# Performance work log

Measured on AMD Instinct MI355X. Metric: run time of the kernel, lower is better.

## Reference

```python
import jax, jax.numpy as jnp
import numpy as np


def _gcn_conv(x, W, b, src, dst, n):
    # PyG GCNConv: add self-loops, symmetric normalization deg^{-1/2} A deg^{-1/2},
    # linear transform, scatter-add aggregation, bias.
    h = x @ W  # [N, H]
    # degree including self-loop (count of dst occurrences + 1)
    deg = jnp.zeros((n,), h.dtype).at[dst].add(1.0) + 1.0
    dinv = jax.lax.rsqrt(deg)  # deg^{-1/2}
    edge_norm = (dinv[src] * dinv[dst])[:, None]  # [E, 1]
    agg = jax.ops.segment_sum(h[src] * edge_norm, dst, num_segments=n)  # [N, H]
    # self-loop contribution: norm = dinv[i]*dinv[i]
    return agg + h * (dinv * dinv)[:, None] + b


def setup_inputs() -> dict:
    N, E, F_IN, HID, OUT = 100000, 1600000, 128, 128, 64
    key = jax.random.key(0)
    ks = jax.random.split(key, 8)
    x = jax.random.normal(ks[0], (N, F_IN), dtype=jnp.float32)
    edge_index = jax.random.randint(ks[1], (2, E), 0, N, dtype=jnp.int32)
    s1 = 1.0 / np.sqrt(F_IN)
    s2 = 1.0 / np.sqrt(HID)
    W1 = jax.random.uniform(ks[2], (F_IN, HID), jnp.float32, -s1, s1)
    b1 = jax.random.uniform(ks[3], (HID,), jnp.float32, -s1, s1)
    W2 = jax.random.uniform(ks[4], (HID, HID), jnp.float32, -s2, s2)
    b2 = jax.random.uniform(ks[5], (HID,), jnp.float32, -s2, s2)
    W_out = jax.random.uniform(ks[6], (HID, OUT), jnp.float32, -s2, s2)
    b_out = jax.random.uniform(ks[7], (OUT,), jnp.float32, -s2, s2)
    return {"x": x, "edge_index": edge_index, "W1": W1, "b1": b1,
            "W2": W2, "b2": b2, "W_out": W_out, "b_out": b_out}


def reference(x, edge_index, W1, b1, W2, b2, W_out, b_out):
    n = x.shape[0]
    src, dst = edge_index[0], edge_index[1]
    h = _gcn_conv(x, W1, b1, src, dst, n)
    h = jax.nn.relu(h)
    # F.dropout(training=self.training): identity in eval mode
    h = _gcn_conv(h, W2, b2, src, dst, n)
    h = jax.nn.relu(h)
    logits = h @ W_out + b_out
    return jax.nn.log_softmax(logits, axis=1)
```

## Files before the change

### kernel.cpp

```cpp
#include <hip/hip_runtime.h>
#include <hip/hip_bf16.h>


#define FEAT 128
#define OUTF 64
#define BSH 7
#define BNODES (1 << BSH)
#define SCHUNK_SH 12
#define SCHUNK (1 << SCHUNK_SH)
#define NREP 8
#define GDEPTH 16

typedef __attribute__((ext_vector_type(8))) short short8;
typedef __attribute__((ext_vector_type(4))) float f32x4;

__device__ __forceinline__ unsigned short bf16_rn(float f) {
    unsigned int u = __float_as_uint(f);
    u += 0x7FFFu + ((u >> 16) & 1u);
    return (unsigned short)(u >> 16);
}
__device__ __forceinline__ float bf16_lo(unsigned int u) { return __uint_as_float(u << 16); }
__device__ __forceinline__ float bf16_hi(unsigned int u) { return __uint_as_float(u & 0xFFFF0000u); }

__global__ __launch_bounds__(256) void bincount8_kernel(
        const int* __restrict__ dst, int* __restrict__ bcnt8, int E, int NB) {
    __shared__ int h[8192];
    int t = threadIdx.x;
    int nb8 = NB * NREP;
    for (int i = t; i < nb8; i += 256) h[i] = 0;
    __syncthreads();
    int stride = gridDim.x * 256;
    for (int e = blockIdx.x * 256 + t; e < E; e += stride) {
        int rep = (e >> SCHUNK_SH) & (NREP - 1);
        atomicAdd(&h[((dst[e] >> BSH) << 3) | rep], 1);
    }
    __syncthreads();
    for (int i = t; i < nb8; i += 256)
        if (h[i]) atomicAdd(&bcnt8[i], h[i]);
}

__global__ __launch_bounds__(1024) void bucket_scan8_kernel(
        const int* __restrict__ bcnt8, int* __restrict__ bcur8,
        int* __restrict__ bbase, int NB, int E) {
    int t = threadIdx.x;
    int nb8 = NB * NREP;
    int base = t * 8;
    int v[8];
    #pragma unroll
    for (int i = 0; i < 8; ++i) v[i] = (base + i < nb8) ? bcnt8[base + i] : 0;
    int local = 0;
    #pragma unroll
    for (int i = 0; i < 8; ++i) local += v[i];
    int lane = t & 63, wv = t >> 6;
    int x = local;
    #pragma unroll
    for (int o = 1; o < 64; o <<= 1) {
        int y = __shfl_up(x, o);
        if (lane >= o) x += y;
    }
    __shared__ int wsum[16];
    if (lane == 63) wsum[wv] = x;
    __syncthreads();
    int woff = 0;
    for (int i = 0; i < wv; ++i) woff += wsum[i];
    int run = woff + x - local;
    #pragma unroll
    for (int i = 0; i < 8; ++i) {
        int g = base + i;
        if (g < nb8) {
            bcur8[g] = run;
            if ((g & (NREP - 1)) == 0) bbase[g >> 3] = run;
        }
        run += v[i];
    }
    if (t == 0) bbase[NB] = E;
}

__global__ __launch_bounds__(256) void bin_scatter_kernel(
        const int* __restrict__ src, const int* __restrict__ dst,
        int* __restrict__ bcur8, unsigned int* __restrict__ staged,
        int E, int NB) {
    __shared__ int lcnt[1024];
    __shared__ int lbase[1024];
    int t = threadIdx.x;
    int rep = blockIdx.x & (NREP - 1);
    int e0 = blockIdx.x << SCHUNK_SH;
    int e1 = min(e0 + SCHUNK, E);
    for (int i = t; i < NB; i += 256) lcnt[i] = 0;
    __syncthreads();
    for (int e = e0 + t; e < e1; e += 256)
        atomicAdd(&lcnt[dst[e] >> BSH], 1);
    __syncthreads();
    for (int i = t; i < NB; i += 256) {
        int c = lcnt[i];
        lbase[i] = c ? atomicAdd(&bcur8[(i << 3) | rep], c) : 0;
        lcnt[i] = 0;
    }
    __syncthreads();
    for (int e = e0 + t; e < e1; e += 256) {
        int s = src[e], d = dst[e];
        int b = d >> BSH, dl = d & (BNODES - 1);
        int pos = lbase[b] + atomicAdd(&lcnt[b], 1);
        staged[pos] = (unsigned int)s | ((unsigned int)dl << 25);
    }
}

__global__ __launch_bounds__(256) void bucket_place_kernel(
        const unsigned int* __restrict__ staged, const int* __restrict__ bbase,
        int* __restrict__ row_ptr, float* __restrict__ dinv,
        int* __restrict__ csr_src, int N, int E) {
    int b = blockIdx.x;
    int t = threadIdx.x;
    int base = bbase[b], end = bbase[b + 1];
    __shared__ int cnt[BNODES];
    __shared__ int cur[BNODES];
    __shared__ int wsum2[2];
    if (t < BNODES) cnt[t] = 0;
    __syncthreads();
    for (int i = base + t; i < end; i += 256)
        atomicAdd(&cnt[staged[i] >> 25], 1);
    __syncthreads();

    bool act = t < BNODES;
    int v = act ? cnt[t] : 0;
    int lane = t & 63, wv = t >> 6;
    int x = v;
    #pragma unroll
    for (int o = 1; o < 64; o <<= 1) {
        int y = __shfl_up(x, o);
        if (lane >= o) x += y;
    }
    if (lane == 63 && wv == 0) wsum2[0] = x;
    __syncthreads();
    if (act) {
        int excl = x - v + (wv == 1 ? wsum2[0] : 0);
        int gnode = b * BNODES + t;
        int rp = base + excl;
        cur[t] = rp;
        if (gnode < N) {
            row_ptr[gnode] = rp;
            dinv[gnode] = rsqrtf((float)v + 1.0f);
        }
    }
    __syncthreads();
    for (int i = base + t; i < end; i += 256) {
        unsigned int u = staged[i];
        int dl = u >> 25;
        int p = atomicAdd(&cur[dl], 1);
        csr_src[p] = (int)(u & 0x1FFFFFFu);
    }
    if (b == 0 && t == 0) row_ptr[N] = E;
}

__global__ __launch_bounds__(256) void convw_kernel(
        const float* __restrict__ W1, const float* __restrict__ W2,
        const float* __restrict__ Wout,
        __hip_bfloat16* __restrict__ W1t, __hip_bfloat16* __restrict__ W2t,
        __hip_bfloat16* __restrict__ WoutT) {
    int idx = blockIdx.x * 256 + threadIdx.x;
    if (idx < 2 * FEAT * FEAT) {
        int which = idx >> 14;
        int r = idx & (FEAT * FEAT - 1);
        int n = r >> 7, k = r & 127;
        const float* W = which ? W2 : W1;
        unsigned short* Wt = (unsigned short*)(which ? W2t : W1t);
        Wt[r] = bf16_rn(W[k * FEAT + n]);
    } else if (idx < 2 * FEAT * FEAT + OUTF * FEAT) {
        int r = idx - 2 * FEAT * FEAT;
        int n = r >> 7, k = r & 127;
        ((unsigned short*)WoutT)[r] = bf16_rn(Wout[k * OUTF + n]);
    }
}

template <bool IN_FP32>
__global__ __launch_bounds__(256) void mfma_gemm_kernel(
        const void* __restrict__ Xv, const __hip_bfloat16* __restrict__ Wt,
        const float* __restrict__ dinv, __hip_bfloat16* __restrict__ Y, int N) {
    __shared__ short Ws[FEAT][136];
    int t = threadIdx.x;
    for (int i = t; i < FEAT * 16; i += 256) {
        int n = i >> 4, c = i & 15;
        *(uint4*)&Ws[n][c * 8] = *(const uint4*)((const unsigned short*)Wt + n * FEAT + c * 8);
    }
    __syncthreads();

    int wave = t >> 6, lane = t & 63;
    int m = lane & 15, quad = lane >> 4;
    int rbase = (blockIdx.x * 4 + wave) * 16;
    if (rbase >= N) return;
    int row = rbase + m;
    bool rok = row < N;

    f32x4 acc[8];
    #pragma unroll
    for (int nt = 0; nt < 8; ++nt) acc[nt] = (f32x4){0.f, 0.f, 0.f, 0.f};

    #pragma unroll
    for (int ks = 0; ks < 4; ++ks) {
        short8 a;
        if (IN_FP32) {
            const float* X = (const float*)Xv;
            float xs[8];
            if (rok) {
                float4 x0 = *(const float4*)(X + (size_t)row * FEAT + ks * 32 + quad * 8);
                float4 x1 = *(const float4*)(X + (size_t)row * FEAT + ks * 32 + quad * 8 + 4);
                xs[0] = x0.x; xs[1] = x0.y; xs[2] = x0.z; xs[3] = x0.w;
                xs[4] = x1.x; xs[5] = x1.y; xs[6] = x1.z; xs[7] = x1.w;
            } else {
                #pragma unroll
                for (int j = 0; j < 8; ++j) xs[j] = 0.f;
            }
            #pragma unroll
            for (int j = 0; j < 8; ++j) a[j] = (short)bf16_rn(xs[j]);
        } else {
            const unsigned short* X = (const unsigned short*)Xv;
            if (rok)
                a = *(const short8*)(X + (size_t)row * FEAT + ks * 32 + quad * 8);
            else {
                #pragma unroll
                for (int j = 0; j < 8; ++j) a[j] = 0;
            }
        }
        #pragma unroll
        for (int nt = 0; nt < 8; ++nt) {
            short8 bfr = *(const short8*)&Ws[nt * 16 + m][ks * 32 + quad * 8];
            acc[nt] = __builtin_amdgcn_mfma_f32_16x16x32_bf16(a, bfr, acc[nt], 0, 0, 0);
        }
    }

    float dr[4];
    #pragma unroll
    for (int r = 0; r < 4; ++r) {
        int ro = rbase + quad * 4 + r;
        dr[r] = (ro < N) ? dinv[ro] : 0.f;
    }
    unsigned short* Yo = (unsigned short*)Y;
    #pragma unroll
    for (int nt = 0; nt < 8; ++nt) {
        #pragma unroll
        for (int r = 0; r < 4; ++r) {
            int ro = rbase + quad * 4 + r;
            if (ro < N)
                Yo[(size_t)ro * FEAT + nt * 16 + m] = bf16_rn(acc[nt][r] * dr[r]);
        }
    }
}

template <int EPI>
__global__ __launch_bounds__(256, 4) void gather_fused_kernel(
        const int* __restrict__ row_ptr, const int* __restrict__ csr_src,
        const float* __restrict__ dinv, const __hip_bfloat16* __restrict__ Hs,
        const float* __restrict__ bias, const __hip_bfloat16* __restrict__ Wt,
        const float* __restrict__ bvec, void* __restrict__ outp, int N) {
    __shared__ short As[16][136];

    int t = threadIdx.x;
    int lane = t & 63;
    int wave = t >> 6;
    int grp = lane >> 4;
    int fl = lane & 15;
    int node = blockIdx.x * 16 + wave * 4 + grp;
    bool nok = node < N;
    int nd = nok ? node : 0;

    const char* Hb = (const char*)Hs;
    unsigned foff = (unsigned)fl << 4;

    uint4 hu = *(const uint4*)(Hb + (((unsigned)nd << 8) + foff));
    float di = dinv[nd];
    float4 b0 = ((const float4*)bias)[fl * 2];
    float4 b1 = ((const float4*)bias)[fl * 2 + 1];

    float acc[8];
    #pragma unroll
    for (int i = 0; i < 8; ++i) acc[i] = 0.f;

    int j = row_ptr[nd], end = row_ptr[nd + 1];

    for (; j + GDEPTH <= end; j += GDEPTH) {
        unsigned off[GDEPTH];
        #pragma unroll
        for (int k = 0; k < GDEPTH; ++k)
            off[k] = ((unsigned)csr_src[j + k] << 8) + foff;
        uint4 u[GDEPTH];
        #pragma unroll
        for (int k = 0; k < GDEPTH; ++k)
            u[k] = *(const uint4*)(Hb + off[k]);
        #pragma unroll
        for (int k = 0; k < GDEPTH; ++k) {
            acc[0] += bf16_lo(u[k].x); acc[1] += bf16_hi(u[k].x);
            acc[2] += bf16_lo(u[k].y); acc[3] += bf16_hi(u[k].y);
            acc[4] += bf16_lo(u[k].z); acc[5] += bf16_hi(u[k].z);
            acc[6] += bf16_lo(u[k].w); acc[7] += bf16_hi(u[k].w);
        }
    }
    if (j < end) {
        int mm = end - j;
        unsigned off[GDEPTH];
        #pragma unroll
        for (int k = 0; k < GDEPTH; ++k)
            off[k] = ((unsigned)csr_src[j + (k < mm ? k : 0)] << 8) + foff;
        uint4 u[GDEPTH];
        #pragma unroll
        for (int k = 0; k < GDEPTH; ++k)
            u[k] = *(const uint4*)(Hb + off[k]);
        #pragma unroll
        for (int k = 0; k < GDEPTH; ++k) {
            if (k < mm) {
                acc[0] += bf16_lo(u[k].x); acc[1] += bf16_hi(u[k].x);
                acc[2] += bf16_lo(u[k].y); acc[3] += bf16_hi(u[k].y);
                acc[4] += bf16_lo(u[k].z); acc[5] += bf16_hi(u[k].z);
                acc[6] += bf16_lo(u[k].w); acc[7] += bf16_hi(u[k].w);
            }
        }
    }

    acc[0] += bf16_lo(hu.x); acc[1] += bf16_hi(hu.x);
    acc[2] += bf16_lo(hu.y); acc[3] += bf16_hi(hu.y);
    acc[4] += bf16_lo(hu.z); acc[5] += bf16_hi(hu.z);
    acc[6] += bf16_lo(hu.w); acc[7] += bf16_hi(hu.w);

    float v0 = fmaxf(di * acc[0] + b0.x, 0.f);
    float v1 = fmaxf(di * acc[1] + b0.y, 0.f);
    float v2 = fmaxf(di * acc[2] + b0.z, 0.f);
    float v3 = fmaxf(di * acc[3] + b0.w, 0.f);
    float v4 = fmaxf(di * acc[4] + b1.x, 0.f);
    float v5 = fmaxf(di * acc[5] + b1.y, 0.f);
    float v6 = fmaxf(di * acc[6] + b1.z, 0.f);
    float v7 = fmaxf(di * acc[7] + b1.w, 0.f);

    uint4 o;
    o.x = (unsigned int)bf16_rn(v0) | ((unsigned int)bf16_rn(v1) << 16);
    o.y = (unsigned int)bf16_rn(v2) | ((unsigned int)bf16_rn(v3) << 16);
    o.z = (unsigned int)bf16_rn(v4) | ((unsigned int)bf16_rn(v5) << 16);
    o.w = (unsigned int)bf16_rn(v6) | ((unsigned int)bf16_rn(v7) << 16);

    *(uint4*)&As[wave * 4 + grp][fl * 8] = o;

    int m = lane & 15, quad = lane >> 4;
    int rbase0 = blockIdx.x * 16;
    const unsigned short* Wu = (const unsigned short*)Wt;

    if (EPI == 1) {
        short8 bf[2][4];
        #pragma unroll
        for (int n2 = 0; n2 < 2; ++n2)
            #pragma unroll
            for (int ks = 0; ks < 4; ++ks)
                bf[n2][ks] = *(const short8*)(
                    Wu + ((wave * 2 + n2) * 16 + m) * FEAT + ks * 32 + quad * 8);
        float dr[4];
        #pragma unroll
        for (int r = 0; r < 4; ++r) {
            int ro = rbase0 + quad * 4 + r;
            dr[r] = (ro < N) ? dinv[ro] : 0.f;
        }
        __syncthreads();
        f32x4 acc2[2];
        #pragma unroll
        for (int n2 = 0; n2 < 2; ++n2) acc2[n2] = (f32x4){0.f, 0.f, 0.f, 0.f};
        #pragma unroll
        for (int ks = 0; ks < 4; ++ks) {
            short8 a = *(const short8*)&As[m][ks * 32 + quad * 8];
            #pragma unroll
            for (int n2 = 0; n2 < 2; ++n2)
                acc2[n2] = __builtin_amdgcn_mfma_f32_16x16x32_bf16(a, bf[n2][ks], acc2[n2], 0, 0, 0);
        }
        unsigned short* Yo = (unsigned short*)outp;
        #pragma unroll
        for (int r = 0; r < 4; ++r) {
            int ro = rbase0 + quad * 4 + r;
            if (ro < N) {
                #pragma unroll
                for (int n2 = 0; n2 < 2; ++n2)
                    Yo[(size_t)ro * FEAT + (wave * 2 + n2) * 16 + m] =
                        bf16_rn(acc2[n2][r] * dr[r]);
            }
        }
    } else {
        short8 bf[4][4];
        float bj[4];
        if (wave == 0) {
            #pragma unroll
            for (int nt = 0; nt < 4; ++nt)
                #pragma unroll
                for (int ks = 0; ks < 4; ++ks)
                    bf[nt][ks] = *(const short8*)(
                        Wu + (nt * 16 + m) * FEAT + ks * 32 + quad * 8);
            #pragma unroll
            for (int nt = 0; nt < 4; ++nt) bj[nt] = bvec[nt * 16 + m];
        }
        __syncthreads();
        if (wave == 0) {
            f32x4 acc4[4];
            #pragma unroll
            for (int nt = 0; nt < 4; ++nt) acc4[nt] = (f32x4){0.f, 0.f, 0.f, 0.f};
            #pragma unroll
            for (int ks = 0; ks < 4; ++ks) {
                short8 a = *(const short8*)&As[m][ks * 32 + quad * 8];
                #pragma unroll
                for (int nt = 0; nt < 4; ++nt)
                    acc4[nt] = __builtin_amdgcn_mfma_f32_16x16x32_bf16(a, bf[nt][ks], acc4[nt], 0, 0, 0);
            }
            float* out = (float*)outp;
            #pragma unroll
            for (int r = 0; r < 4; ++r) {
                int ro = rbase0 + quad * 4 + r;
                if (ro >= N) continue;
                float w0 = acc4[0][r] + bj[0];
                float w1 = acc4[1][r] + bj[1];
                float w2 = acc4[2][r] + bj[2];
                float w3 = acc4[3][r] + bj[3];
                float mx = fmaxf(fmaxf(w0, w1), fmaxf(w2, w3));
                #pragma unroll
                for (int os = 1; os <= 8; os <<= 1) mx = fmaxf(mx, __shfl_xor(mx, os));
                float s = __expf(w0 - mx) + __expf(w1 - mx) + __expf(w2 - mx) + __expf(w3 - mx);
                #pragma unroll
                for (int os = 1; os <= 8; os <<= 1) s += __shfl_xor(s, os);
                float ls = mx + __logf(s);
                float* op = out + (size_t)ro * OUTF + m;
                op[0]  = w0 - ls;
                op[16] = w1 - ls;
                op[32] = w2 - ls;
                op[48] = w3 - ls;
            }
        }
    }
}

extern "C" void kernel_launch(void* const* d_in, const int* in_sizes, int n_in,
                              void* d_out, int out_size, void* d_ws, size_t ws_size,
                              hipStream_t stream) {
    const float* x    = (const float*)d_in[0];
    const int*   ei   = (const int*)  d_in[1];
    const float* W1   = (const float*)d_in[2];
    const float* b1   = (const float*)d_in[3];
    const float* W2   = (const float*)d_in[4];
    const float* b2   = (const float*)d_in[5];
    const float* Wout = (const float*)d_in[6];
    const float* bout = (const float*)d_in[7];
    float* out = (float*)d_out;

    int N = in_sizes[0] / FEAT;
    int E = in_sizes[1] / 2;
    const int* srcp = ei;
    const int* dstp = ei + E;
    int NB = (N + BNODES - 1) >> BSH;

    char* ws = (char*)d_ws;
    __hip_bfloat16* Bh   = (__hip_bfloat16*)ws;
    __hip_bfloat16* Ba   = Bh + (size_t)N * FEAT;
    __hip_bfloat16* W1t  = Ba + (size_t)N * FEAT;
    __hip_bfloat16* W2t  = W1t + FEAT * FEAT;
    __hip_bfloat16* WoutT = W2t + FEAT * FEAT;
    float* dinv    = (float*)(WoutT + OUTF * FEAT);
    int*   rowp    = (int*)(dinv + N);
    int*   bcnt8   = rowp + N + 1;
    int*   bcur8   = bcnt8 + 8192;
    int*   bbase   = bcur8 + 8192;
    unsigned int* staged = (unsigned int*)(bbase + 1032);
    int*   csrsrc  = (int*)(staged + E);

    hipMemsetAsync(bcnt8, 0, (size_t)NB * NREP * sizeof(int), stream);
    bincount8_kernel<<<256, 256, 0, stream>>>(dstp, bcnt8, E, NB);
    bucket_scan8_kernel<<<1, 1024, 0, stream>>>(bcnt8, bcur8, bbase, NB, E);
    bin_scatter_kernel<<<(E + SCHUNK - 1) / SCHUNK, 256, 0, stream>>>(
        srcp, dstp, bcur8, staged, E, NB);
    bucket_place_kernel<<<NB, 256, 0, stream>>>(staged, bbase, rowp, dinv, csrsrc, N, E);
    convw_kernel<<<(2 * FEAT * FEAT + OUTF * FEAT + 255) / 256, 256, 0, stream>>>(
        W1, W2, Wout, W1t, W2t, WoutT);

    int ggrid = (N + 63) / 64;
    int agrid = (N + 15) / 16;

    mfma_gemm_kernel<true><<<ggrid, 256, 0, stream>>>(x, W1t, dinv, Bh, N);

    gather_fused_kernel<1><<<agrid, 256, 0, stream>>>(
        rowp, csrsrc, dinv, Bh, b1, W2t, nullptr, Ba, N);

    gather_fused_kernel<2><<<agrid, 256, 0, stream>>>(
        rowp, csrsrc, dinv, Ba, b2, WoutT, bout, out, N);
}
```

Before: 316.7 us.

## Sort nodes by degree and process gather in degree order for load balance

Builds a degree histogram during CSR placement, scans it, and creates a permutation of nodes grouped by in-degree. The two fused gather kernels then process nodes in that permuted order, so the lanes in a wave handle nodes of similar degree and less time is lost to divergence. The memset is folded into the weight-conversion kernel. In exchange the change adds two small kernels and a histogram pass, and the output writes and row accesses become scattered rather than contiguous.

Measured after the change: 424.3 us. +34.0%, slower.

```diff
diff --git a/kernel.cpp b/kernel.cpp
--- a/kernel.cpp
+++ b/kernel.cpp
@@ -22,142 +22,19 @@
 __device__ __forceinline__ float bf16_lo(unsigned int u) { return __uint_as_float(u << 16); }
 __device__ __forceinline__ float bf16_hi(unsigned int u) { return __uint_as_float(u & 0xFFFF0000u); }
 
-__global__ __launch_bounds__(256) void bincount8_kernel(
-        const int* __restrict__ dst, int* __restrict__ bcnt8, int E, int NB) {
-    __shared__ int h[8192];
-    int t = threadIdx.x;
-    int nb8 = NB * NREP;
-    for (int i = t; i < nb8; i += 256) h[i] = 0;
-    __syncthreads();
-    int stride = gridDim.x * 256;
-    for (int e = blockIdx.x * 256 + t; e < E; e += stride) {
-        int rep = (e >> SCHUNK_SH) & (NREP - 1);
-        atomicAdd(&h[((dst[e] >> BSH) << 3) | rep], 1);
-    }
-    __syncthreads();
-    for (int i = t; i < nb8; i += 256)
-        if (h[i]) atomicAdd(&bcnt8[i], h[i]);
-}
-
-__global__ __launch_bounds__(1024) void bucket_scan8_kernel(
-        const int* __restrict__ bcnt8, int* __restrict__ bcur8,
-        int* __restrict__ bbase, int NB, int E) {
-    int t = threadIdx.x;
-    int nb8 = NB * NREP;
-    int base = t * 8;
-    int v[8];
-    #pragma unroll
-    for (int i = 0; i < 8; ++i) v[i] = (base + i < nb8) ? bcnt8[base + i] : 0;
-    int local = 0;
-    #pragma unroll
-    for (int i = 0; i < 8; ++i) local += v[i];
-    int lane = t & 63, wv = t >> 6;
-    int x = local;
-    #pragma unroll
-    for (int o = 1; o < 64; o <<= 1) {
-        int y = __shfl_up(x, o);
-        if (lane >= o) x += y;
-    }
-    __shared__ int wsum[16];
-    if (lane == 63) wsum[wv] = x;
-    __syncthreads();
-    int woff = 0;
-    for (int i = 0; i < wv; ++i) woff += wsum[i];
-    int run = woff + x - local;
-    #pragma unroll
-    for (int i = 0; i < 8; ++i) {
-        int g = base + i;
-        if (g < nb8) {
-            bcur8[g] = run;
-            if ((g & (NREP - 1)) == 0) bbase[g >> 3] = run;
-        }
-        run += v[i];
-    }
-    if (t == 0) bbase[NB] = E;
-}
-
-__global__ __launch_bounds__(256) void bin_scatter_kernel(
-        const int* __restrict__ src, const int* __restrict__ dst,
-        int* __restrict__ bcur8, unsigned int* __restrict__ staged,
-        int E, int NB) {
-    __shared__ int lcnt[1024];
-    __shared__ int lbase[1024];
-    int t = threadIdx.x;
-    int rep = blockIdx.x & (NREP - 1);
-    int e0 = blockIdx.x << SCHUNK_SH;
-    int e1 = min(e0 + SCHUNK, E);
-    for (int i = t; i < NB; i += 256) lcnt[i] = 0;
-    __syncthreads();
-    for (int e = e0 + t; e < e1; e += 256)
-        atomicAdd(&lcnt[dst[e] >> BSH], 1);
-    __syncthreads();
-    for (int i = t; i < NB; i += 256) {
-        int c = lcnt[i];
-        lbase[i] = c ? atomicAdd(&bcur8[(i << 3) | rep], c) : 0;
-        lcnt[i] = 0;
-    }
-    __syncthreads();
-    for (int e = e0 + t; e < e1; e += 256) {
-        int s = src[e], d = dst[e];
-        int b = d >> BSH, dl = d & (BNODES - 1);
-        int pos = lbase[b] + atomicAdd(&lcnt[b], 1);
-        staged[pos] = (unsigned int)s | ((unsigned int)dl << 25);
-    }
-}
-
-__global__ __launch_bounds__(256) void bucket_place_kernel(
-        const unsigned int* __restrict__ staged, const int* __restrict__ bbase,
-        int* __restrict__ row_ptr, float* __restrict__ dinv,
-        int* __restrict__ csr_src, int N, int E) {
-    int b = blockIdx.x;
-    int t = threadIdx.x;
-    int base = bbase[b], end = bbase[b + 1];
-    __shared__ int cnt[BNODES];
-    __shared__ int cur[BNODES];
-    __shared__ int wsum2[2];
-    if (t < BNODES) cnt[t] = 0;
-    __syncthreads();
-    for (int i = base + t; i < end; i += 256)
-        atomicAdd(&cnt[staged[i] >> 25], 1);
-    __syncthreads();
-
-    bool act = t < BNODES;
-    int v = act ? cnt[t] : 0;
-    int lane = t & 63, wv = t >> 6;
-    int x = v;
-    #pragma unroll
-    for (int o = 1; o < 64; o <<= 1) {
-        int y = __shfl_up(x, o);
-        if (lane >= o) x += y;
-    }
-    if (lane == 63 && wv == 0) wsum2[0] = x;
-    __syncthreads();
-    if (act) {
-        int excl = x - v + (wv == 1 ? wsum2[0] : 0);
-        int gnode = b * BNODES + t;
-        int rp = base + excl;
-        cur[t] = rp;
-        if (gnode < N) {
-            row_ptr[gnode] = rp;
-            dinv[gnode] = rsqrtf((float)v + 1.0f);
-        }
-    }
-    __syncthreads();
-    for (int i = base + t; i < end; i += 256) {
-        unsigned int u = staged[i];
-        int dl = u >> 25;
-        int p = atomicAdd(&cur[dl], 1);
-        csr_src[p] = (int)(u & 0x1FFFFFFu);
-    }
-    if (b == 0 && t == 0) row_ptr[N] = E;
-}
-
 __global__ __launch_bounds__(256) void convw_kernel(
         const float* __restrict__ W1, const float* __restrict__ W2,
         const float* __restrict__ Wout,
         __hip_bfloat16* __restrict__ W1t, __hip_bfloat16* __restrict__ W2t,
-        __hip_bfloat16* __restrict__ WoutT) {
-    int idx = blockIdx.x * 256 + threadIdx.x;
+        __hip_bfloat16* __restrict__ WoutT,
+        int* __restrict__ bcnt8, int* __restrict__ dhist8) {
+    int bx = blockIdx.x;
+    if (bx >= 160) {
+        int* z = (bx < 192) ? dhist8 : bcnt8;
+        z[((bx & 31) << 8) | threadIdx.x] = 0;
+        return;
+    }
+    int idx = bx * 256 + threadIdx.x;
     if (idx < 2 * FEAT * FEAT) {
         int which = idx >> 14;
         int r = idx & (FEAT * FEAT - 1);
@@ -172,6 +49,183 @@
     }
 }
 
+__global__ __launch_bounds__(256) void bincount8_kernel(
+        const int* __restrict__ dst, int* __restrict__ bcnt8, int E, int NB) {
+    __shared__ int h[8192];
+    int t = threadIdx.x;
+    int nb8 = NB * NREP;
+    for (int i = t; i < nb8; i += 256) h[i] = 0;
+    __syncthreads();
+    int stride = gridDim.x * 256;
+    for (int e = blockIdx.x * 256 + t; e < E; e += stride) {
+        int rep = (e >> SCHUNK_SH) & (NREP - 1);
+        atomicAdd(&h[((dst[e] >> BSH) << 3) | rep], 1);
+    }
+    __syncthreads();
+    for (int i = t; i < nb8; i += 256)
+        if (h[i]) atomicAdd(&bcnt8[i], h[i]);
+}
+
+__global__ __launch_bounds__(1024) void bucket_scan8_kernel(
+        const int* __restrict__ bcnt8, int* __restrict__ bcur8,
+        int* __restrict__ bbase, int NB, int E) {
+    int t = threadIdx.x;
+    int nb8 = NB * NREP;
+    int base = t * 8;
+    int v[8];
+    #pragma unroll
+    for (int i = 0; i < 8; ++i) v[i] = (base + i < nb8) ? bcnt8[base + i] : 0;
+    int local = 0;
+    #pragma unroll
+    for (int i = 0; i < 8; ++i) local += v[i];
+    int lane = t & 63, wv = t >> 6;
+    int x = local;
+    #pragma unroll
+    for (int o = 1; o < 64; o <<= 1) {
+        int y = __shfl_up(x, o);
+        if (lane >= o) x += y;
+    }
+    __shared__ int wsum[16];
+    if (lane == 63) wsum[wv] = x;
+    __syncthreads();
+    int woff = 0;
+    for (int i = 0; i < wv; ++i) woff += wsum[i];
+    int run = woff + x - local;
+    #pragma unroll
+    for (int i = 0; i < 8; ++i) {
+        int g = base + i;
+        if (g < nb8) {
+            bcur8[g] = run;
+            if ((g & (NREP - 1)) == 0) bbase[g >> 3] = run;
+        }
+        run += v[i];
+    }
+    if (t == 0) bbase[NB] = E;
+}
+
+__global__ __launch_bounds__(256) void bin_scatter_kernel(
+        const int* __restrict__ src, const int* __restrict__ dst,
+        int* __restrict__ bcur8, unsigned int* __restrict__ staged,
+        int E, int NB) {
+    __shared__ int lcnt[1024];
+    __shared__ int lbase[1024];
+    int t = threadIdx.x;
+    int rep = blockIdx.x & (NREP - 1);
+    int e0 = blockIdx.x << SCHUNK_SH;
+    int e1 = min(e0 + SCHUNK, E);
+    for (int i = t; i < NB; i += 256) lcnt[i] = 0;
+    __syncthreads();
+    for (int e = e0 + t; e < e1; e += 256)
+        atomicAdd(&lcnt[dst[e] >> BSH], 1);
+    __syncthreads();
+    for (int i = t; i < NB; i += 256) {
+        int c = lcnt[i];
+        lbase[i] = c ? atomicAdd(&bcur8[(i << 3) | rep], c) : 0;
+        lcnt[i] = 0;
+    }
+    __syncthreads();
+    for (int e = e0 + t; e < e1; e += 256) {
+        int s = src[e], d = dst[e];
+        int b = d >> BSH, dl = d & (BNODES - 1);
+        int pos = lbase[b] + atomicAdd(&lcnt[b], 1);
+        staged[pos] = (unsigned int)s | ((unsigned int)dl << 25);
+    }
+}
+
+__global__ __launch_bounds__(256) void bucket_place_kernel(
+        const unsigned int* __restrict__ staged, const int* __restrict__ bbase,
+        int* __restrict__ row_ptr, float* __restrict__ dinv,
+        int* __restrict__ csr_src, int* __restrict__ dhist8, int N, int E) {
+    int b = blockIdx.x;
+    int t = threadIdx.x;
+    int base = bbase[b], end = bbase[b + 1];
+    __shared__ int cnt[BNODES];
+    __shared__ int cur[BNODES];
+    __shared__ int dh[256];
+    __shared__ int wsum2[2];
+    if (t < BNODES) cnt[t] = 0;
+    dh[t] = 0;
+    __syncthreads();
+    for (int i = base + t; i < end; i += 256)
+        atomicAdd(&cnt[staged[i] >> 25], 1);
+    __syncthreads();
+
+    bool act = t < BNODES;
+    int v = act ? cnt[t] : 0;
+    int lane = t & 63, wv = t >> 6;
+    int x = v;
+    #pragma unroll
+    for (int o = 1; o < 64; o <<= 1) {
+        int y = __shfl_up(x, o);
+        if (lane >= o) x += y;
+    }
+    if (lane == 63 && wv == 0) wsum2[0] = x;
+    __syncthreads();
+    if (act) {
+        int excl = x - v + (wv == 1 ? wsum2[0] : 0);
+        int gnode = b * BNODES + t;
+        int rp = base + excl;
+        cur[t] = rp;
+        if (gnode < N) {
+            row_ptr[gnode] = rp;
+            dinv[gnode] = rsqrtf((float)v + 1.0f);
+            atomicAdd(&dh[min(v, 255)], 1);
+        }
+    }
+    __syncthreads();
+    for (int i = base + t; i < end; i += 256) {
+        unsigned int u = staged[i];
+        int dl = u >> 25;
+        int p = atomicAdd(&cur[dl], 1);
+        csr_src[p] = (int)(u & 0x1FFFFFFu);
+    }
+    int rr = b & 31;
+    if (dh[t]) atomicAdd(&dhist8[(t << 5) | rr], dh[t]);
+    if (b == 0 && t == 0) row_ptr[N] = E;
+}
+
+__global__ __launch_bounds__(1024) void scanD_kernel(
+        const int* __restrict__ dh8, int* __restrict__ dcur8) {
+    int t = threadIdx.x;
+    int base = t * 8;
+    int v[8];
+    #pragma unroll
+    for (int i = 0; i < 8; ++i) v[i] = dh8[base + i];
+    int local = 0;
+    #pragma unroll
+    for (int i = 0; i < 8; ++i) local += v[i];
+    int lane = t & 63, wv = t >> 6;
+    int x = local;
+    #pragma unroll
+    for (int o = 1; o < 64; o <<= 1) {
+        int y = __shfl_up(x, o);
+        if (lane >= o) x += y;
+    }
+    __shared__ int wsum[16];
+    if (lane == 63) wsum[wv] = x;
+    __syncthreads();
+    int woff = 0;
+    for (int i = 0; i < wv; ++i) woff += wsum[i];
+    int run = woff + x - local;
+    #pragma unroll
+    for (int i = 0; i < 8; ++i) {
+        dcur8[base + i] = run;
+        run += v[i];
+    }
+}
+
+__global__ __launch_bounds__(128) void dperm_kernel(
+        const int* __restrict__ row_ptr, int* __restrict__ dcur8,
+        int* __restrict__ perm, int N) {
+    int b = blockIdx.x;
+    int node = b * BNODES + threadIdx.x;
+    if (node < N) {
+        int dc = min(row_ptr[node + 1] - row_ptr[node], 255);
+        int p = atomicAdd(&dcur8[(dc << 5) | (b & 31)], 1);
+        perm[p] = node;
+    }
+}
+
 template <bool IN_FP32>
 __global__ __launch_bounds__(256) void mfma_gemm_kernel(
         const void* __restrict__ Xv, const __hip_bfloat16* __restrict__ Wt,
@@ -251,7 +305,8 @@
         const int* __restrict__ row_ptr, const int* __restrict__ csr_src,
         const float* __restrict__ dinv, const __hip_bfloat16* __restrict__ Hs,
         const float* __restrict__ bias, const __hip_bfloat16* __restrict__ Wt,
-        const float* __restrict__ bvec, void* __restrict__ outp, int N) {
+        const float* __restrict__ bvec, const int* __restrict__ perm,
+        void* __restrict__ outp, int N) {
     __shared__ short As[16][136];
 
     int t = threadIdx.x;
@@ -259,9 +314,9 @@
     int wave = t >> 6;
     int grp = lane >> 4;
     int fl = lane & 15;
-    int node = blockIdx.x * 16 + wave * 4 + grp;
-    bool nok = node < N;
-    int nd = nok ? node : 0;
+    int po = blockIdx.x * 16 + wave * 4 + grp;
+    bool nok = po < N;
+    int nd = nok ? perm[po] : 0;
 
     const char* Hb = (const char*)Hs;
     unsigned foff = (unsigned)fl << 4;
@@ -349,11 +404,13 @@
             for (int ks = 0; ks < 4; ++ks)
                 bf[n2][ks] = *(const short8*)(
                     Wu + ((wave * 2 + n2) * 16 + m) * FEAT + ks * 32 + quad * 8);
+        int ror[4];
         float dr[4];
         #pragma unroll
         for (int r = 0; r < 4; ++r) {
-            int ro = rbase0 + quad * 4 + r;
-            dr[r] = (ro < N) ? dinv[ro] : 0.f;
+            int p2 = rbase0 + quad * 4 + r;
+            ror[r] = (p2 < N) ? perm[p2] : -1;
+            dr[r] = (ror[r] >= 0) ? dinv[ror[r]] : 0.f;
         }
         __syncthreads();
         f32x4 acc2[2];
@@ -369,17 +426,17 @@
         unsigned short* Yo = (unsigned short*)outp;
         #pragma unroll
         for (int r = 0; r < 4; ++r) {
-            int ro = rbase0 + quad * 4 + r;
-            if (ro < N) {
+            if (ror[r] >= 0) {
                 #pragma unroll
                 for (int n2 = 0; n2 < 2; ++n2)
-                    Yo[(size_t)ro * FEAT + (wave * 2 + n2) * 16 + m] =
+                    Yo[(size_t)ror[r] * FEAT + (wave * 2 + n2) * 16 + m] =
                         bf16_rn(acc2[n2][r] * dr[r]);
             }
         }
     } else {
         short8 bf[4][4];
         float bj[4];
+        int ror[4];
         if (wave == 0) {
             #pragma unroll
             for (int nt = 0; nt < 4; ++nt)
@@ -389,6 +446,11 @@
                         Wu + (nt * 16 + m) * FEAT + ks * 32 + quad * 8);
             #pragma unroll
             for (int nt = 0; nt < 4; ++nt) bj[nt] = bvec[nt * 16 + m];
+            #pragma unroll
+            for (int r = 0; r < 4; ++r) {
+                int p2 = rbase0 + quad * 4 + r;
+                ror[r] = (p2 < N) ? perm[p2] : -1;
+            }
         }
         __syncthreads();
         if (wave == 0) {
@@ -405,8 +467,7 @@
             float* out = (float*)outp;
             #pragma unroll
             for (int r = 0; r < 4; ++r) {
-                int ro = rbase0 + quad * 4 + r;
-                if (ro >= N) continue;
+                if (ror[r] < 0) continue;
                 float w0 = acc4[0][r] + bj[0];
                 float w1 = acc4[1][r] + bj[1];
                 float w2 = acc4[2][r] + bj[2];
@@ -418,7 +479,7 @@
                 #pragma unroll
                 for (int os = 1; os <= 8; os <<= 1) s += __shfl_xor(s, os);
                 float ls = mx + __logf(s);
-                float* op = out + (size_t)ro * OUTF + m;
+                float* op = out + (size_t)ror[r] * OUTF + m;
                 op[0]  = w0 - ls;
                 op[16] = w1 - ls;
                 op[32] = w2 - ls;
@@ -458,17 +519,22 @@
     int*   bcnt8   = rowp + N + 1;
     int*   bcur8   = bcnt8 + 8192;
     int*   bbase   = bcur8 + 8192;
-    unsigned int* staged = (unsigned int*)(bbase + 1032);
+    int*   dhist8  = bbase + 1032;
+    int*   dcur8   = dhist8 + 8192;
+    int*   perm    = dcur8 + 8192;
+    unsigned int* staged = (unsigned int*)(perm + N);
     int*   csrsrc  = (int*)(staged + E);
 
-    hipMemsetAsync(bcnt8, 0, (size_t)NB * NREP * sizeof(int), stream);
+    convw_kernel<<<224, 256, 0, stream>>>(
+        W1, W2, Wout, W1t, W2t, WoutT, bcnt8, dhist8);
     bincount8_kernel<<<256, 256, 0, stream>>>(dstp, bcnt8, E, NB);
     bucket_scan8_kernel<<<1, 1024, 0, stream>>>(bcnt8, bcur8, bbase, NB, E);
     bin_scatter_kernel<<<(E + SCHUNK - 1) / SCHUNK, 256, 0, stream>>>(
         srcp, dstp, bcur8, staged, E, NB);
-    bucket_place_kernel<<<NB, 256, 0, stream>>>(staged, bbase, rowp, dinv, csrsrc, N, E);
-    convw_kernel<<<(2 * FEAT * FEAT + OUTF * FEAT + 255) / 256, 256, 0, stream>>>(
-        W1, W2, Wout, W1t, W2t, WoutT);
+    bucket_place_kernel<<<NB, 256, 0, stream>>>(
+        staged, bbase, rowp, dinv, csrsrc, dhist8, N, E);
+    scanD_kernel<<<1, 1024, 0, stream>>>(dhist8, dcur8);
+    dperm_kernel<<<NB, 128, 0, stream>>>(rowp, dcur8, perm, N);
 
     int ggrid = (N + 63) / 64;
     int agrid = (N + 15) / 16;
@@ -476,8 +542,8 @@
     mfma_gemm_kernel<true><<<ggrid, 256, 0, stream>>>(x, W1t, dinv, Bh, N);
 
     gather_fused_kernel<1><<<agrid, 256, 0, stream>>>(
-        rowp, csrsrc, dinv, Bh, b1, W2t, nullptr, Ba, N);
+        rowp, csrsrc, dinv, Bh, b1, W2t, nullptr, perm, Ba, N);
 
     gather_fused_kernel<2><<<agrid, 256, 0, stream>>>(
-        rowp, csrsrc, dinv, Ba, b2, WoutT, bout, out, N);
-}
+        rowp, csrsrc, dinv, Ba, b2, WoutT, bout, perm, out, N);
+}
```
